# Performance work log

Hardware: AMD Instinct MI355X
Metric: run time of the kernel (lower is better)

The kernel has to match this reference:

```python
import jax, jax.numpy as jnp
import numpy as np

B, S = 2, 2048
HID, NH, NKV, HD = 4096, 32, 8, 128
THETA = 10000.0
WINDOW = 1024  # sliding window size


def setup_inputs() -> dict:
    key = jax.random.key(0)
    k1, k2, k3 = jax.random.split(key, 3)
    hidden_states = jax.random.normal(k1, (B, S, HID), jnp.float32)
    wqkv = jax.random.normal(k2, (HID, (NH + 2 * NKV) * HD), jnp.float32) * 0.02
    wo = jax.random.normal(k3, (NH * HD, HID), jnp.float32) * 0.02
    positions = jnp.arange(S, dtype=jnp.int32)
    return {"hidden_states": hidden_states, "wqkv": wqkv, "wo": wo, "positions": positions}


def _rope_neox(x, positions):
    # x: [B, S, h, HD]; GPT-NeoX style: rotate concatenated halves.
    half = HD // 2
    inv_freq = 1.0 / (THETA ** (jnp.arange(half, dtype=jnp.float32) / half))
    ang = positions.astype(jnp.float32)[:, None] * inv_freq  # [S, half]
    cos = jnp.cos(ang)[None, :, None, :]
    sin = jnp.sin(ang)[None, :, None, :]
    x1, x2 = jnp.split(x, 2, axis=-1)
    return jnp.concatenate([x1 * cos - x2 * sin, x2 * cos + x1 * sin], axis=-1)


def reference(hidden_states, wqkv, wo, positions):
    qkv = hidden_states @ wqkv  # [B, S, (NH+2*NKV)*HD]
    q, k, v = jnp.split(qkv, [NH * HD, NH * HD + NKV * HD], axis=-1)
    q = q.reshape(B, S, NH, HD)
    k = k.reshape(B, S, NKV, HD)
    v = v.reshape(B, S, NKV, HD)
    q = _rope_neox(q, positions)
    k = _rope_neox(k, positions)
    # GQA: each KV head serves NH // NKV query heads
    rep = NH // NKV
    k = jnp.repeat(k, rep, axis=2)  # [B, S, NH, HD]
    v = jnp.repeat(v, rep, axis=2)
    scale = HD ** -0.5
    scores = jnp.einsum('bqhd,bkhd->bhqk', q, k) * scale  # [B, NH, S, S]
    i = jnp.arange(S)[:, None]
    j = jnp.arange(S)[None, :]
    mask = (j <= i) & (i - j < WINDOW)  # causal + sliding window
    scores = jnp.where(mask[None, None], scores, jnp.float32(-1e30))
    probs = jax.nn.softmax(scores, axis=-1)
    attn = jnp.einsum('bhqk,bkhd->bqhd', probs, v).reshape(B, S, NH * HD)
    return attn @ wo  # [B, S, HID]
```

## Files before the change

kernel.cpp:

```cpp
#include <hip/hip_runtime.h>


typedef __attribute__((ext_vector_type(8))) short short8;
typedef __attribute__((ext_vector_type(4))) float f32x4;
typedef __attribute__((ext_vector_type(16))) float f32x16;
typedef __attribute__((ext_vector_type(4))) unsigned int u32x4;
typedef __attribute__((ext_vector_type(4))) unsigned short u16x4;

__device__ __forceinline__ unsigned short f2bf(float f) {
  unsigned int u = __builtin_bit_cast(unsigned int, f);
  u = u + 0x7fffu + ((u >> 16) & 1u);
  return (unsigned short)(u >> 16);
}
__device__ __forceinline__ float bf2f(unsigned short h) {
  unsigned int u = ((unsigned int)h) << 16;
  return __builtin_bit_cast(float, u);
}
__device__ __forceinline__ unsigned int cvtpk_bf16(float lo, float hi) {
  unsigned int r;
  asm("v_cvt_pk_bf16_f32 %0, %1, %2" : "=v"(r) : "v"(lo), "v"(hi));
  return r;
}

__device__ __forceinline__ void gload_lds16(const unsigned short* g, unsigned short* l) {
  __builtin_amdgcn_global_load_lds(
      (const __attribute__((address_space(1))) unsigned int*)g,
      (__attribute__((address_space(3))) unsigned int*)l, 16, 0, 0);
}

#define MFMA16(A, B, C) __builtin_amdgcn_mfma_f32_16x16x32_bf16((A), (B), (C), 0, 0, 0)
#define MFMA32(A, B, C) __builtin_amdgcn_mfma_f32_32x32x16_bf16((A), (B), (C), 0, 0, 0)
#define BC8(x) __builtin_bit_cast(short8, (x))

__global__ __launch_bounds__(256) void cvt1(const float* __restrict__ hs,
                                            const float* __restrict__ wqkv,
                                            unsigned short* __restrict__ hsb,
                                            unsigned short* __restrict__ wT) {
  const int bid = blockIdx.x;
  if (bid < 24576) {
    __shared__ float t[32][33];
    const int c0 = (bid % 192) * 32, r0 = (bid / 192) * 32;
    const int tx = threadIdx.x & 31, ty = threadIdx.x >> 5;
#pragma unroll
    for (int i = 0; i < 4; ++i)
      t[ty + i * 8][tx] = wqkv[(size_t)(r0 + ty + i * 8) * 6144 + c0 + tx];
    __syncthreads();
#pragma unroll
    for (int i = 0; i < 4; ++i)
      wT[(size_t)(c0 + ty + i * 8) * 4096 + r0 + tx] = f2bf(t[tx][ty + i * 8]);
  } else {
    const int i = ((bid - 24576) * 256 + threadIdx.x) * 4;
    f32x4 v = *(const f32x4*)(hs + i);
    u16x4 o;
#pragma unroll
    for (int j = 0; j < 4; ++j) o[j] = f2bf(v[j]);
    *(u16x4*)(hsb + i) = o;
  }
}

__global__ __launch_bounds__(256) void rope_cvtwo(unsigned short* __restrict__ qkv,
                                                  const int* __restrict__ pos,
                                                  const float* __restrict__ wo,
                                                  unsigned short* __restrict__ wT) {
  const int bid = blockIdx.x;
  if (bid < 8192) {
    const int idx = bid * 256 + threadIdx.x;
    const int d = idx & 63;
    const int hh = (idx >> 6) & 7;
    const int tok = idx >> 9;
    const int s = tok & 2047;
    unsigned short* p = qkv + (size_t)tok * 6144 + 4096 + hh * 128 + d;
    const float x1 = bf2f(p[0]);
    const float x2 = bf2f(p[64]);
    const float inv = exp2f(-(float)d * 0.2076205059304601f);
    const float ang = (float)pos[s] * inv;
    const float c = cosf(ang), sn = sinf(ang);
    p[0]  = f2bf(x1 * c - x2 * sn);
    p[64] = f2bf(x2 * c + x1 * sn);
  } else {
    __shared__ float t[32][33];
    const int b2 = bid - 8192;
    const int c0 = (b2 % 128) * 32, r0 = (b2 / 128) * 32;
    const int tx = threadIdx.x & 31, ty = threadIdx.x >> 5;
#pragma unroll
    for (int i = 0; i < 4; ++i)
      t[ty + i * 8][tx] = wo[(size_t)(r0 + ty + i * 8) * 4096 + c0 + tx];
    __syncthreads();
#pragma unroll
    for (int i = 0; i < 4; ++i)
      wT[(size_t)(c0 + ty + i * 8) * 4096 + r0 + tx] = f2bf(t[tx][ty + i * 8]);
  }
}

template <int NIF, int OUTF32>
__global__ __launch_bounds__(512, 2) void gemm256(const unsigned short* __restrict__ A,
                                                  const unsigned short* __restrict__ BT,
                                                  void* __restrict__ Cout,
                                                  int M, int N, int K) {
  constexpr int BUFE = 16384 + NIF * 4096;
  constexpr int NR = NIF + 4;
  __shared__ __align__(16) unsigned short lds[2][BUFE];
  const int tid = threadIdx.x;
  const int lane = tid & 63;
  const int w = tid >> 6;
  const int wr = w >> 2;
  const int wc = w & 3;
  const int g = lane >> 4;
  const int l15 = lane & 15;

  const int nwg = gridDim.x;
  const int cpx = nwg >> 3;
  const int bid = blockIdx.x;
  const int swz = (bid & 7) * cpx + (bid >> 3);
  const int MT = M >> 8;
  const int m0 = (swz % MT) * 256;
  const int n0 = (swz / MT) * (NIF * 64);

  const int lrow = lane >> 3;
  const int lcol = ((lane & 7) ^ lrow) * 8;
  const unsigned short* Asrc = A + (size_t)(m0 + w * 8 + lrow) * K + lcol;
  const unsigned short* Bsrc = BT + (size_t)(n0 + w * 8 + lrow) * K + lcol;

  f32x4 acc[8][NIF] = {};

  auto stage = [&](int buf, int t, int r) {
    if (r < NIF) {
      const int rb = r * 64;
      gload_lds16(Bsrc + (size_t)rb * K + t * 64,
                  &lds[buf][16384 + (rb + w * 8) * 64]);
    } else {
      const int j = r - NIF;
      const int rb = (j & 1) * 128 + ((j >> 1) & 1) * 64;
      gload_lds16(Asrc + (size_t)rb * K + t * 64,
                  &lds[buf][(rb + w * 8) * 64]);
    }
  };
  auto rdA = [&](int buf, int mi, int ks) {
    const int row = wr * 128 + mi * 16 + l15;
    const int cb = (ks * 64 + g * 16) ^ ((l15 & 7) << 4);
    return *(const u32x4*)((const char*)&lds[buf][0] + row * 128 + cb);
  };
  auto rdB = [&](int buf, int ni, int ks) {
    const int row = wc * (NIF * 16) + ni * 16 + l15;
    const int cb = (ks * 64 + g * 16) ^ ((l15 & 7) << 4);
    return *(const u32x4*)((const char*)&lds[buf][0] + 32768 + row * 128 + cb);
  };

#pragma unroll
  for (int r = 0; r < NR; ++r) stage(0, 0, r);
  asm volatile("s_waitcnt vmcnt(2)" ::: "memory");
  __builtin_amdgcn_s_barrier();

  const int NT = K >> 6;
  for (int t = 0; t < NT; ++t) {
    const int cb_ = t & 1, nb_ = cb_ ^ 1;
    const bool pre = (t + 1 < NT);
    u32x4 bfr[NIF][2];

    {
#pragma unroll
      for (int ni = 0; ni < NIF; ++ni) {
        bfr[ni][0] = rdB(cb_, ni, 0);
        bfr[ni][1] = rdB(cb_, ni, 1);
      }
      u32x4 af[3][2];
#pragma unroll
      for (int mi = 0; mi < 3; ++mi) {
        af[mi][0] = rdA(cb_, mi, 0);
        af[mi][1] = rdA(cb_, mi, 1);
      }
      if (pre) {
        stage(nb_, t + 1, 0); stage(nb_, t + 1, 1);
        if (NIF == 4) stage(nb_, t + 1, 2);
        asm volatile("s_waitcnt vmcnt(%0)" :: "i"(NIF == 4 ? 3 : 2) : "memory");
      } else {
        asm volatile("s_waitcnt vmcnt(0)" ::: "memory");
      }
      __builtin_amdgcn_s_barrier();
      __builtin_amdgcn_s_setprio(1);
#pragma unroll
      for (int mi = 0; mi < 3; ++mi)
#pragma unroll
        for (int ni = 0; ni < NIF; ++ni) {
          acc[mi][ni] = MFMA16(BC8(af[mi][0]), BC8(bfr[ni][0]), acc[mi][ni]);
          acc[mi][ni] = MFMA16(BC8(af[mi][1]), BC8(bfr[ni][1]), acc[mi][ni]);
        }
      __builtin_amdgcn_s_setprio(0);
      __builtin_amdgcn_s_barrier();
    }
    {
      u32x4 af[3][2];
#pragma unroll
      for (int mi = 0; mi < 3; ++mi) {
        af[mi][0] = rdA(cb_, 3 + mi, 0);
        af[mi][1] = rdA(cb_, 3 + mi, 1);
      }
      if (pre) {
        stage(nb_, t + 1, NR - 5); stage(nb_, t + 1, NR - 4); stage(nb_, t + 1, NR - 3);
      }
      __builtin_amdgcn_s_barrier();
      __builtin_amdgcn_s_setprio(1);
#pragma unroll
      for (int mi = 0; mi < 3; ++mi)
#pragma unroll
        for (int ni = 0; ni < NIF; ++ni) {
          acc[3 + mi][ni] = MFMA16(BC8(af[mi][0]), BC8(bfr[ni][0]), acc[3 + mi][ni]);
          acc[3 + mi][ni] = MFMA16(BC8(af[mi][1]), BC8(bfr[ni][1]), acc[3 + mi][ni]);
        }
      __builtin_amdgcn_s_setprio(0);
      __builtin_amdgcn_s_barrier();
    }
    {
      u32x4 af[2][2];
#pragma unroll
      for (int mi = 0; mi < 2; ++mi) {
        af[mi][0] = rdA(cb_, 6 + mi, 0);
        af[mi][1] = rdA(cb_, 6 + mi, 1);
      }
      if (pre) {
        stage(nb_, t + 1, NR - 2); stage(nb_, t + 1, NR - 1);
        asm volatile("s_waitcnt vmcnt(2)" ::: "memory");
      }
      __builtin_amdgcn_s_barrier();
      __builtin_amdgcn_s_setprio(1);
#pragma unroll
      for (int mi = 0; mi < 2; ++mi)
#pragma unroll
        for (int ni = 0; ni < NIF; ++ni) {
          acc[6 + mi][ni] = MFMA16(BC8(af[mi][0]), BC8(bfr[ni][0]), acc[6 + mi][ni]);
          acc[6 + mi][ni] = MFMA16(BC8(af[mi][1]), BC8(bfr[ni][1]), acc[6 + mi][ni]);
        }
      __builtin_amdgcn_s_setprio(0);
      __builtin_amdgcn_s_barrier();
    }
  }

  const int crow0 = m0 + wr * 128;
  const int ccol0 = n0 + wc * (NIF * 16);
#pragma unroll
  for (int mi = 0; mi < 8; ++mi)
#pragma unroll
    for (int ni = 0; ni < NIF; ++ni)
#pragma unroll
      for (int r = 0; r < 4; ++r) {
        const size_t idx =
            (size_t)(crow0 + mi * 16 + g * 4 + r) * N + (ccol0 + ni * 16 + l15);
        if constexpr (OUTF32) ((float*)Cout)[idx] = acc[mi][ni][r];
        else ((unsigned short*)Cout)[idx] = f2bf(acc[mi][ni][r]);
      }
}

__global__ __launch_bounds__(512, 2) void attn_kernel(const unsigned short* __restrict__ qkv,
                                                      unsigned short* __restrict__ aout,
                                                      const int* __restrict__ pos) {
  __shared__ __align__(16) unsigned short smem[35840];

  const int tid = threadIdx.x;
  const int lane = tid & 63;
  const int w = tid >> 6;
  const int hi = lane >> 5;
  const int l31 = lane & 31;
  const int q0 = blockIdx.x * 256;
  const int h = blockIdx.y;
  const int b = blockIdx.z;
  const int kh = h >> 2;
  const size_t tokbase = (size_t)b * 2048;
  const int qw0 = q0 + w * 32;
  const int qg = qw0 + l31;

  short8 qf[8];
  {
    const unsigned short* qp = qkv + (tokbase + qg) * 6144 + h * 128;
#pragma unroll
    for (int ks8 = 0; ks8 < 8; ++ks8)
      qf[ks8] = BC8(*(const u32x4*)(qp + ks8 * 16 + hi * 8));
    const float fp = (float)pos[qg];
#pragma unroll
    for (int ks8 = 0; ks8 < 4; ++ks8)
#pragma unroll
      for (int j = 0; j < 8; ++j) {
        const int d = ks8 * 16 + hi * 8 + j;
        const float x1 = bf2f((unsigned short)qf[ks8][j]);
        const float x2 = bf2f((unsigned short)qf[ks8 + 4][j]);
        const float ang = fp * exp2f(-(float)d * 0.2076205059304601f);
        float c, sn;
        __sincosf(ang, &sn, &c);
        c *= 0.12751743f; sn *= 0.12751743f;
        qf[ks8][j]     = (short)f2bf(x1 * c - x2 * sn);
        qf[ks8 + 4][j] = (short)f2bf(x2 * c + x1 * sn);
      }
  }

  const int c0key = tid >> 4, c0col = tid & 15;
  const int c1key = (tid + 512) >> 4, c1col = tid & 15;

  u32x4 kreg[2], vreg[2];
  const unsigned short* kvK = qkv + tokbase * 6144 + 4096 + kh * 128;

  const int t0 = (q0 >= 1024 ? (q0 - 1023) >> 6 : 0);
  const int t1 = (q0 + 255) >> 6;

  {
    const unsigned short* kb = kvK + (size_t)(t0 * 64) * 6144;
    kreg[0] = *(const u32x4*)(kb + (size_t)c0key * 6144 + c0col * 8);
    kreg[1] = *(const u32x4*)(kb + (size_t)c1key * 6144 + c1col * 8);
    vreg[0] = *(const u32x4*)(kb + (size_t)c0key * 6144 + 1024 + c0col * 8);
    vreg[1] = *(const u32x4*)(kb + (size_t)c1key * 6144 + 1024 + c1col * 8);
  }

  float m_run = -1e30f, l_run = 0.0f;
  f32x16 o_acc[4] = {};

  for (int kt = t0; kt <= t1; ++kt) {
    const int cur = (kt - t0) & 1;
    unsigned short* kdst = &smem[(cur)*17920];
    unsigned short* vdst = kdst + 8704;

    if (kt == t0) {
      *(u32x4*)&kdst[c0key * 136 + c0col * 8] = kreg[0];
      *(u32x4*)&kdst[c1key * 136 + c1col * 8] = kreg[1];
#pragma unroll
      for (int e = 0; e < 8; ++e) {
        const int e0 = (e + c0col) & 7;
        const int e1 = (e + c1col) & 7;
        vdst[(c0col * 8 + e0) * 72 + c0key] =
            (unsigned short)(vreg[0][e0 >> 1] >> ((e0 & 1) * 16));
        vdst[(c1col * 8 + e1) * 72 + c1key] =
            (unsigned short)(vreg[1][e1 >> 1] >> ((e1 & 1) * 16));
      }
      if (kt < t1) {
        const unsigned short* kb = kvK + (size_t)((kt + 1) * 64) * 6144;
        kreg[0] = *(const u32x4*)(kb + (size_t)c0key * 6144 + c0col * 8);
        kreg[1] = *(const u32x4*)(kb + (size_t)c1key * 6144 + c1col * 8);
        vreg[0] = *(const u32x4*)(kb + (size_t)c0key * 6144 + 1024 + c0col * 8);
        vreg[1] = *(const u32x4*)(kb + (size_t)c1key * 6144 + 1024 + c1col * 8);
      }
      __syncthreads();
    }

    if (kt < t1) {
      unsigned short* kdn = &smem[(cur ^ 1) * 17920];
      unsigned short* vdn = kdn + 8704;
      *(u32x4*)&kdn[c0key * 136 + c0col * 8] = kreg[0];
      *(u32x4*)&kdn[c1key * 136 + c1col * 8] = kreg[1];
#pragma unroll
      for (int e = 0; e < 8; ++e) {
        const int e0 = (e + c0col) & 7;
        const int e1 = (e + c1col) & 7;
        vdn[(c0col * 8 + e0) * 72 + c0key] =
            (unsigned short)(vreg[0][e0 >> 1] >> ((e0 & 1) * 16));
        vdn[(c1col * 8 + e1) * 72 + c1key] =
            (unsigned short)(vreg[1][e1 >> 1] >> ((e1 & 1) * 16));
      }
      if (kt + 2 <= t1) {
        const unsigned short* kb = kvK + (size_t)((kt + 2) * 64) * 6144;
        kreg[0] = *(const u32x4*)(kb + (size_t)c0key * 6144 + c0col * 8);
        kreg[1] = *(const u32x4*)(kb + (size_t)c1key * 6144 + c1col * 8);
        vreg[0] = *(const u32x4*)(kb + (size_t)c0key * 6144 + 1024 + c0col * 8);
        vreg[1] = *(const u32x4*)(kb + (size_t)c1key * 6144 + 1024 + c1col * 8);
      }
    }

    const int ktb = kt * 64;
    if (ktb <= qw0 + 31 && ktb + 63 >= qw0 - 1023) {
      const unsigned short* kb = &smem[cur * 17920];
      const unsigned short* vb = kb + 8704;

      f32x16 s0 = {}, s1 = {};
      const int arow = l31 * 136 + hi * 8;
#pragma unroll
      for (int ks8 = 0; ks8 < 8; ++ks8) {
        u32x4 a0 = *(const u32x4*)&kb[arow + ks8 * 16];
        u32x4 a1 = *(const u32x4*)&kb[arow + 32 * 136 + ks8 * 16];
        s0 = MFMA32(BC8(a0), qf[ks8], s0);
        s1 = MFMA32(BC8(a1), qf[ks8], s1);
      }

      float pv[32];
      const bool need_mask = !(ktb + 63 <= qw0 && ktb >= qw0 - 992);
      if (need_mask) {
#pragma unroll
        for (int r = 0; r < 16; ++r) {
          const int key0 = ktb + ((r & 3) + 8 * (r >> 2) + 4 * hi);
          const int key1 = key0 + 32;
          pv[r]      = (key0 <= qg && qg - key0 < 1024) ? s0[r] : -1e30f;
          pv[16 + r] = (key1 <= qg && qg - key1 < 1024) ? s1[r] : -1e30f;
        }
      } else {
#pragma unroll
        for (int r = 0; r < 16; ++r) {
          pv[r] = s0[r];
          pv[16 + r] = s1[r];
        }
      }

      float tm = -1e30f;
#pragma unroll
      for (int i = 0; i < 32; ++i) tm = fmaxf(tm, pv[i]);
      tm = fmaxf(tm, __shfl_xor(tm, 32, 64));
      if (__any(tm > m_run + 11.5415603f)) {
        const float mn = fmaxf(fmaxf(m_run, tm), -1e20f);
        const float scl = exp2f(m_run - mn);
#pragma unroll
        for (int d = 0; d < 4; ++d) o_acc[d] *= scl;
        l_run *= scl;
        m_run = mn;
      }
      float lsum = 0.0f;
#pragma unroll
      for (int i = 0; i < 32; ++i) {
        pv[i] = exp2f(pv[i] - m_run);
        lsum += pv[i];
      }
      l_run += lsum + __shfl_xor(lsum, 32, 64);

      u32x4 paf[4];
#pragma unroll
      for (int ks = 0; ks < 4; ++ks) {
        const int base = (ks >> 1) * 16 + (ks & 1) * 8;
        auto rA = __builtin_amdgcn_permlane32_swap(
            (int)cvtpk_bf16(pv[base + 0], pv[base + 1]),
            (int)cvtpk_bf16(pv[base + 4], pv[base + 5]), false, false);
        auto rB = __builtin_amdgcn_permlane32_swap(
            (int)cvtpk_bf16(pv[base + 2], pv[base + 3]),
            (int)cvtpk_bf16(pv[base + 6], pv[base + 7]), false, false);
        paf[ks][0] = (unsigned int)rA[0];
        paf[ks][1] = (unsigned int)rB[0];
        paf[ks][2] = (unsigned int)rA[1];
        paf[ks][3] = (unsigned int)rB[1];
      }

#pragma unroll
      for (int dblk = 0; dblk < 4; ++dblk) {
        const int vrow = (dblk * 32 + l31) * 72 + hi * 8;
#pragma unroll
        for (int ks = 0; ks < 4; ++ks) {
          u32x4 vf = *(const u32x4*)&vb[vrow + ks * 16];
          o_acc[dblk] = MFMA32(BC8(vf), BC8(paf[ks]), o_acc[dblk]);
        }
      }
    }

    __syncthreads();
  }

  const float rl = 1.0f / l_run;
  unsigned short* ob = &smem[w * 4352];
#pragma unroll
  for (int dblk = 0; dblk < 4; ++dblk)
#pragma unroll
    for (int rq = 0; rq < 4; ++rq) {
      u16x4 pk;
#pragma unroll
      for (int i = 0; i < 4; ++i) pk[i] = f2bf(o_acc[dblk][rq * 4 + i] * rl);
      *(u16x4*)&ob[l31 * 136 + dblk * 32 + rq * 8 + hi * 4] = pk;
    }
  __syncthreads();

  unsigned short* gout = aout + (tokbase + q0 + w * 32) * 4096 + h * 128;
#pragma unroll
  for (int r4 = 0; r4 < 8; ++r4) {
    const int row = r4 * 4 + (lane >> 4);
    u32x4 val = *(const u32x4*)&ob[row * 136 + (lane & 15) * 8];
    *(u32x4*)(gout + (size_t)row * 4096 + (lane & 15) * 8) = val;
  }
}

extern "C" void kernel_launch(void* const* d_in, const int* in_sizes, int n_in,
                              void* d_out, int out_size, void* d_ws, size_t ws_size,
                              hipStream_t stream) {
  (void)in_sizes; (void)n_in; (void)out_size; (void)ws_size;
  const float* hs   = (const float*)d_in[0];
  const float* wqkv = (const float*)d_in[1];
  const float* wo   = (const float*)d_in[2];
  const int*   pos  = (const int*)d_in[3];
  float* out = (float*)d_out;

  char* ws = (char*)d_ws;
  unsigned short* qkvb = (unsigned short*)ws;
  unsigned short* wT   = (unsigned short*)(ws + 50331648);
  unsigned short* hsb  = (unsigned short*)(ws + 100663296);

  cvt1<<<40960, 256, 0, stream>>>(hs, wqkv, hsb, wT);
  gemm256<3, 0><<<512, 512, 0, stream>>>(hsb, wT, qkvb, 4096, 6144, 4096);
  rope_cvtwo<<<24576, 256, 0, stream>>>(qkvb, pos, wo, wT);
  attn_kernel<<<dim3(8, 32, 2), 512, 0, stream>>>(qkvb, hsb, pos);
  gemm256<4, 1><<<256, 512, 0, stream>>>(hsb, wT, out, 4096, 4096, 4096);
}
```

Baseline: 489.0 us.

## Split GEMM into simple-sync and 4-phase pipelined variants, use natural-exp softmax

The single gemm256 template becomes two kernels. gemm_ss is used for the QKV projection: it waits for all loads, stages the whole next tile up front, and uses fewer barriers. gemm_p4 is used for the output projection: it splits each K-step into four phases of two M-subtiles, interleaving staged global loads with sched_barrier fences and explicit lgkmcnt waits. The attention kernel drops the folded log2e/sqrt(d) scale from the query RoPE and instead multiplies scores by 1/sqrt(d) and uses __expf with a rescale threshold of 8. The simpler sync in gemm_ss gives up load/compute overlap, and the extra per-score multiply adds ALU work in attention.

```diff
diff --git a/kernel.cpp b/kernel.cpp
--- a/kernel.cpp
+++ b/kernel.cpp
@@ -93,7 +93,7 @@
 }
 
 template <int NIF, int OUTF32>
-__global__ __launch_bounds__(512, 2) void gemm256(const unsigned short* __restrict__ A,
+__global__ __launch_bounds__(512, 2) void gemm_ss(const unsigned short* __restrict__ A,
                                                   const unsigned short* __restrict__ BT,
                                                   void* __restrict__ Cout,
                                                   int M, int N, int K) {
@@ -148,7 +148,154 @@
 
 #pragma unroll
   for (int r = 0; r < NR; ++r) stage(0, 0, r);
+
+  const int NT = K >> 6;
+  for (int t = 0; t < NT; ++t) {
+    const int cb_ = t & 1, nb_ = cb_ ^ 1;
+
+    asm volatile("s_waitcnt vmcnt(0)" ::: "memory");
+    __builtin_amdgcn_s_barrier();
+    asm volatile("" ::: "memory");
+    if (t + 1 < NT) {
+#pragma unroll
+      for (int r = 0; r < NR; ++r) stage(nb_, t + 1, r);
+    }
+
+    u32x4 bfr[NIF][2];
+#pragma unroll
+    for (int ni = 0; ni < NIF; ++ni) {
+      bfr[ni][0] = rdB(cb_, ni, 0);
+      bfr[ni][1] = rdB(cb_, ni, 1);
+    }
+
+    {
+      u32x4 af[3][2];
+#pragma unroll
+      for (int mi = 0; mi < 3; ++mi) {
+        af[mi][0] = rdA(cb_, mi, 0);
+        af[mi][1] = rdA(cb_, mi, 1);
+      }
+      __builtin_amdgcn_s_setprio(1);
+#pragma unroll
+      for (int mi = 0; mi < 3; ++mi)
+#pragma unroll
+        for (int ni = 0; ni < NIF; ++ni) {
+          acc[mi][ni] = MFMA16(BC8(af[mi][0]), BC8(bfr[ni][0]), acc[mi][ni]);
+          acc[mi][ni] = MFMA16(BC8(af[mi][1]), BC8(bfr[ni][1]), acc[mi][ni]);
+        }
+      __builtin_amdgcn_s_setprio(0);
+    }
+    __builtin_amdgcn_s_barrier();
+    {
+      u32x4 af[3][2];
+#pragma unroll
+      for (int mi = 0; mi < 3; ++mi) {
+        af[mi][0] = rdA(cb_, 3 + mi, 0);
+        af[mi][1] = rdA(cb_, 3 + mi, 1);
+      }
+      __builtin_amdgcn_s_setprio(1);
+#pragma unroll
+      for (int mi = 0; mi < 3; ++mi)
+#pragma unroll
+        for (int ni = 0; ni < NIF; ++ni) {
+          acc[3 + mi][ni] = MFMA16(BC8(af[mi][0]), BC8(bfr[ni][0]), acc[3 + mi][ni]);
+          acc[3 + mi][ni] = MFMA16(BC8(af[mi][1]), BC8(bfr[ni][1]), acc[3 + mi][ni]);
+        }
+      __builtin_amdgcn_s_setprio(0);
+    }
+    __builtin_amdgcn_s_barrier();
+    {
+      u32x4 af[2][2];
+#pragma unroll
+      for (int mi = 0; mi < 2; ++mi) {
+        af[mi][0] = rdA(cb_, 6 + mi, 0);
+        af[mi][1] = rdA(cb_, 6 + mi, 1);
+      }
+      __builtin_amdgcn_s_setprio(1);
+#pragma unroll
+      for (int mi = 0; mi < 2; ++mi)
+#pragma unroll
+        for (int ni = 0; ni < NIF; ++ni) {
+          acc[6 + mi][ni] = MFMA16(BC8(af[mi][0]), BC8(bfr[ni][0]), acc[6 + mi][ni]);
+          acc[6 + mi][ni] = MFMA16(BC8(af[mi][1]), BC8(bfr[ni][1]), acc[6 + mi][ni]);
+        }
+      __builtin_amdgcn_s_setprio(0);
+    }
+  }
+
+  const int crow0 = m0 + wr * 128;
+  const int ccol0 = n0 + wc * (NIF * 16);
+#pragma unroll
+  for (int mi = 0; mi < 8; ++mi)
+#pragma unroll
+    for (int ni = 0; ni < NIF; ++ni)
+#pragma unroll
+      for (int r = 0; r < 4; ++r) {
+        const size_t idx =
+            (size_t)(crow0 + mi * 16 + g * 4 + r) * N + (ccol0 + ni * 16 + l15);
+        if constexpr (OUTF32) ((float*)Cout)[idx] = acc[mi][ni][r];
+        else ((unsigned short*)Cout)[idx] = f2bf(acc[mi][ni][r]);
+      }
+}
+
+template <int NIF, int OUTF32>
+__global__ __launch_bounds__(512, 2) void gemm_p4(const unsigned short* __restrict__ A,
+                                                  const unsigned short* __restrict__ BT,
+                                                  void* __restrict__ Cout,
+                                                  int M, int N, int K) {
+  constexpr int BUFE = 16384 + NIF * 4096;
+  constexpr int NR = NIF + 4;
+  __shared__ __align__(16) unsigned short lds[2][BUFE];
+  const int tid = threadIdx.x;
+  const int lane = tid & 63;
+  const int w = tid >> 6;
+  const int wr = w >> 2;
+  const int wc = w & 3;
+  const int g = lane >> 4;
+  const int l15 = lane & 15;
+
+  const int nwg = gridDim.x;
+  const int cpx = nwg >> 3;
+  const int bid = blockIdx.x;
+  const int swz = (bid & 7) * cpx + (bid >> 3);
+  const int MT = M >> 8;
+  const int m0 = (swz % MT) * 256;
+  const int n0 = (swz / MT) * (NIF * 64);
+
+  const int lrow = lane >> 3;
+  const int lcol = ((lane & 7) ^ lrow) * 8;
+  const unsigned short* Asrc = A + (size_t)(m0 + w * 8 + lrow) * K + lcol;
+  const unsigned short* Bsrc = BT + (size_t)(n0 + w * 8 + lrow) * K + lcol;
+
+  f32x4 acc[8][NIF] = {};
+
+  auto stage = [&](int buf, int t, int r) {
+    if (r < NIF) {
+      const int rb = r * 64;
+      gload_lds16(Bsrc + (size_t)rb * K + t * 64,
+                  &lds[buf][16384 + (rb + w * 8) * 64]);
+    } else {
+      const int j = r - NIF;
+      const int rb = (j & 1) * 128 + ((j >> 1) & 1) * 64;
+      gload_lds16(Asrc + (size_t)rb * K + t * 64,
+                  &lds[buf][(rb + w * 8) * 64]);
+    }
+  };
+  auto rdA = [&](int buf, int mi, int ks) {
+    const int row = wr * 128 + mi * 16 + l15;
+    const int cb = (ks * 64 + g * 16) ^ ((l15 & 7) << 4);
+    return *(const u32x4*)((const char*)&lds[buf][0] + row * 128 + cb);
+  };
+  auto rdB = [&](int buf, int ni, int ks) {
+    const int row = wc * (NIF * 16) + ni * 16 + l15;
+    const int cb = (ks * 64 + g * 16) ^ ((l15 & 7) << 4);
+    return *(const u32x4*)((const char*)&lds[buf][0] + 32768 + row * 128 + cb);
+  };
+
+#pragma unroll
+  for (int r = 0; r < NR; ++r) stage(0, 0, r);
   asm volatile("s_waitcnt vmcnt(2)" ::: "memory");
+  __builtin_amdgcn_sched_barrier(0);
   __builtin_amdgcn_s_barrier();
 
   const int NT = K >> 6;
@@ -163,74 +310,92 @@
         bfr[ni][0] = rdB(cb_, ni, 0);
         bfr[ni][1] = rdB(cb_, ni, 1);
       }
-      u32x4 af[3][2];
-#pragma unroll
-      for (int mi = 0; mi < 3; ++mi) {
-        af[mi][0] = rdA(cb_, mi, 0);
-        af[mi][1] = rdA(cb_, mi, 1);
-      }
+      u32x4 a00 = rdA(cb_, 0, 0), a01 = rdA(cb_, 0, 1);
+      u32x4 a10 = rdA(cb_, 1, 0), a11 = rdA(cb_, 1, 1);
+      if (pre) { stage(nb_, t + 1, 0); stage(nb_, t + 1, 1); }
+      __builtin_amdgcn_sched_barrier(0);
+      __builtin_amdgcn_s_barrier();
+      asm volatile("s_waitcnt lgkmcnt(0)" ::: "memory");
+      __builtin_amdgcn_sched_barrier(0);
+      __builtin_amdgcn_s_setprio(1);
+#pragma unroll
+      for (int ni = 0; ni < NIF; ++ni) {
+        acc[0][ni] = MFMA16(BC8(a00), BC8(bfr[ni][0]), acc[0][ni]);
+        acc[0][ni] = MFMA16(BC8(a01), BC8(bfr[ni][1]), acc[0][ni]);
+        acc[1][ni] = MFMA16(BC8(a10), BC8(bfr[ni][0]), acc[1][ni]);
+        acc[1][ni] = MFMA16(BC8(a11), BC8(bfr[ni][1]), acc[1][ni]);
+      }
+      __builtin_amdgcn_s_setprio(0);
+      __builtin_amdgcn_sched_barrier(0);
+      __builtin_amdgcn_s_barrier();
+    }
+    {
+      u32x4 a00 = rdA(cb_, 2, 0), a01 = rdA(cb_, 2, 1);
+      u32x4 a10 = rdA(cb_, 3, 0), a11 = rdA(cb_, 3, 1);
       if (pre) {
-        stage(nb_, t + 1, 0); stage(nb_, t + 1, 1);
-        if (NIF == 4) stage(nb_, t + 1, 2);
-        asm volatile("s_waitcnt vmcnt(%0)" :: "i"(NIF == 4 ? 3 : 2) : "memory");
+        stage(nb_, t + 1, 2); stage(nb_, t + 1, 3);
+        asm volatile("s_waitcnt vmcnt(4)" ::: "memory");
       } else {
         asm volatile("s_waitcnt vmcnt(0)" ::: "memory");
       }
-      __builtin_amdgcn_s_barrier();
+      __builtin_amdgcn_sched_barrier(0);
+      __builtin_amdgcn_s_barrier();
+      asm volatile("s_waitcnt lgkmcnt(0)" ::: "memory");
+      __builtin_amdgcn_sched_barrier(0);
       __builtin_amdgcn_s_setprio(1);
 #pragma unroll
-      for (int mi = 0; mi < 3; ++mi)
-#pragma unroll
-        for (int ni = 0; ni < NIF; ++ni) {
-          acc[mi][ni] = MFMA16(BC8(af[mi][0]), BC8(bfr[ni][0]), acc[mi][ni]);
-          acc[mi][ni] = MFMA16(BC8(af[mi][1]), BC8(bfr[ni][1]), acc[mi][ni]);
-        }
+      for (int ni = 0; ni < NIF; ++ni) {
+        acc[2][ni] = MFMA16(BC8(a00), BC8(bfr[ni][0]), acc[2][ni]);
+        acc[2][ni] = MFMA16(BC8(a01), BC8(bfr[ni][1]), acc[2][ni]);
+        acc[3][ni] = MFMA16(BC8(a10), BC8(bfr[ni][0]), acc[3][ni]);
+        acc[3][ni] = MFMA16(BC8(a11), BC8(bfr[ni][1]), acc[3][ni]);
+      }
       __builtin_amdgcn_s_setprio(0);
+      __builtin_amdgcn_sched_barrier(0);
       __builtin_amdgcn_s_barrier();
     }
     {
-      u32x4 af[3][2];
-#pragma unroll
-      for (int mi = 0; mi < 3; ++mi) {
-        af[mi][0] = rdA(cb_, 3 + mi, 0);
-        af[mi][1] = rdA(cb_, 3 + mi, 1);
-      }
+      u32x4 a00 = rdA(cb_, 4, 0), a01 = rdA(cb_, 4, 1);
+      u32x4 a10 = rdA(cb_, 5, 0), a11 = rdA(cb_, 5, 1);
+      if (pre) { stage(nb_, t + 1, 4); stage(nb_, t + 1, 5); }
+      __builtin_amdgcn_sched_barrier(0);
+      __builtin_amdgcn_s_barrier();
+      asm volatile("s_waitcnt lgkmcnt(0)" ::: "memory");
+      __builtin_amdgcn_sched_barrier(0);
+      __builtin_amdgcn_s_setprio(1);
+#pragma unroll
+      for (int ni = 0; ni < NIF; ++ni) {
+        acc[4][ni] = MFMA16(BC8(a00), BC8(bfr[ni][0]), acc[4][ni]);
+        acc[4][ni] = MFMA16(BC8(a01), BC8(bfr[ni][1]), acc[4][ni]);
+        acc[5][ni] = MFMA16(BC8(a10), BC8(bfr[ni][0]), acc[5][ni]);
+        acc[5][ni] = MFMA16(BC8(a11), BC8(bfr[ni][1]), acc[5][ni]);
+      }
+      __builtin_amdgcn_s_setprio(0);
+      __builtin_amdgcn_sched_barrier(0);
+      __builtin_amdgcn_s_barrier();
+    }
+    {
+      u32x4 a00 = rdA(cb_, 6, 0), a01 = rdA(cb_, 6, 1);
+      u32x4 a10 = rdA(cb_, 7, 0), a11 = rdA(cb_, 7, 1);
       if (pre) {
-        stage(nb_, t + 1, NR - 5); stage(nb_, t + 1, NR - 4); stage(nb_, t + 1, NR - 3);
-      }
-      __builtin_amdgcn_s_barrier();
+        stage(nb_, t + 1, 6);
+        if (NR == 8) stage(nb_, t + 1, 7);
+        asm volatile("s_waitcnt vmcnt(2)" ::: "memory");
+      }
+      __builtin_amdgcn_sched_barrier(0);
+      __builtin_amdgcn_s_barrier();
+      asm volatile("s_waitcnt lgkmcnt(0)" ::: "memory");
+      __builtin_amdgcn_sched_barrier(0);
       __builtin_amdgcn_s_setprio(1);
 #pragma unroll
-      for (int mi = 0; mi < 3; ++mi)
-#pragma unroll
-        for (int ni = 0; ni < NIF; ++ni) {
-          acc[3 + mi][ni] = MFMA16(BC8(af[mi][0]), BC8(bfr[ni][0]), acc[3 + mi][ni]);
-          acc[3 + mi][ni] = MFMA16(BC8(af[mi][1]), BC8(bfr[ni][1]), acc[3 + mi][ni]);
-        }
+      for (int ni = 0; ni < NIF; ++ni) {
+        acc[6][ni] = MFMA16(BC8(a00), BC8(bfr[ni][0]), acc[6][ni]);
+        acc[6][ni] = MFMA16(BC8(a01), BC8(bfr[ni][1]), acc[6][ni]);
+        acc[7][ni] = MFMA16(BC8(a10), BC8(bfr[ni][0]), acc[7][ni]);
+        acc[7][ni] = MFMA16(BC8(a11), BC8(bfr[ni][1]), acc[7][ni]);
+      }
       __builtin_amdgcn_s_setprio(0);
-      __builtin_amdgcn_s_barrier();
-    }
-    {
-      u32x4 af[2][2];
-#pragma unroll
-      for (int mi = 0; mi < 2; ++mi) {
-        af[mi][0] = rdA(cb_, 6 + mi, 0);
-        af[mi][1] = rdA(cb_, 6 + mi, 1);
-      }
-      if (pre) {
-        stage(nb_, t + 1, NR - 2); stage(nb_, t + 1, NR - 1);
-        asm volatile("s_waitcnt vmcnt(2)" ::: "memory");
-      }
-      __builtin_amdgcn_s_barrier();
-      __builtin_amdgcn_s_setprio(1);
-#pragma unroll
-      for (int mi = 0; mi < 2; ++mi)
-#pragma unroll
-        for (int ni = 0; ni < NIF; ++ni) {
-          acc[6 + mi][ni] = MFMA16(BC8(af[mi][0]), BC8(bfr[ni][0]), acc[6 + mi][ni]);
-          acc[6 + mi][ni] = MFMA16(BC8(af[mi][1]), BC8(bfr[ni][1]), acc[6 + mi][ni]);
-        }
-      __builtin_amdgcn_s_setprio(0);
+      __builtin_amdgcn_sched_barrier(0);
       __builtin_amdgcn_s_barrier();
     }
   }
@@ -285,7 +450,6 @@
         const float ang = fp * exp2f(-(float)d * 0.2076205059304601f);
         float c, sn;
         __sincosf(ang, &sn, &c);
-        c *= 0.12751743f; sn *= 0.12751743f;
         qf[ks8][j]     = (short)f2bf(x1 * c - x2 * sn);
         qf[ks8 + 4][j] = (short)f2bf(x2 * c + x1 * sn);
       }
@@ -376,6 +540,7 @@
         s1 = MFMA32(BC8(a1), qf[ks8], s1);
       }
 
+      const float scale = 0.08838834764831845f;
       float pv[32];
       const bool need_mask = !(ktb + 63 <= qw0 && ktb >= qw0 - 992);
       if (need_mask) {
@@ -383,14 +548,14 @@
         for (int r = 0; r < 16; ++r) {
           const int key0 = ktb + ((r & 3) + 8 * (r >> 2) + 4 * hi);
           const int key1 = key0 + 32;
-          pv[r]      = (key0 <= qg && qg - key0 < 1024) ? s0[r] : -1e30f;
-          pv[16 + r] = (key1 <= qg && qg - key1 < 1024) ? s1[r] : -1e30f;
+          pv[r]      = (key0 <= qg && qg - key0 < 1024) ? s0[r] * scale : -1e30f;
+          pv[16 + r] = (key1 <= qg && qg - key1 < 1024) ? s1[r] * scale : -1e30f;
         }
       } else {
 #pragma unroll
         for (int r = 0; r < 16; ++r) {
-          pv[r] = s0[r];
-          pv[16 + r] = s1[r];
+          pv[r] = s0[r] * scale;
+          pv[16 + r] = s1[r] * scale;
         }
       }
 
@@ -398,9 +563,9 @@
 #pragma unroll
       for (int i = 0; i < 32; ++i) tm = fmaxf(tm, pv[i]);
       tm = fmaxf(tm, __shfl_xor(tm, 32, 64));
-      if (__any(tm > m_run + 11.5415603f)) {
+      if (__any(tm > m_run + 8.0f)) {
         const float mn = fmaxf(fmaxf(m_run, tm), -1e20f);
-        const float scl = exp2f(m_run - mn);
+        const float scl = __expf(m_run - mn);
 #pragma unroll
         for (int d = 0; d < 4; ++d) o_acc[d] *= scl;
         l_run *= scl;
@@ -409,7 +574,7 @@
       float lsum = 0.0f;
 #pragma unroll
       for (int i = 0; i < 32; ++i) {
-        pv[i] = exp2f(pv[i] - m_run);
+        pv[i] = __expf(pv[i] - m_run);
         lsum += pv[i];
       }
       l_run += lsum + __shfl_xor(lsum, 32, 64);
@@ -482,8 +647,8 @@
   unsigned short* hsb  = (unsigned short*)(ws + 100663296);
 
   cvt1<<<40960, 256, 0, stream>>>(hs, wqkv, hsb, wT);
-  gemm256<3, 0><<<512, 512, 0, stream>>>(hsb, wT, qkvb, 4096, 6144, 4096);
+  gemm_ss<3, 0><<<512, 512, 0, stream>>>(hsb, wT, qkvb, 4096, 6144, 4096);
   rope_cvtwo<<<24576, 256, 0, stream>>>(qkvb, pos, wo, wT);
   attn_kernel<<<dim3(8, 32, 2), 512, 0, stream>>>(qkvb, hsb, pos);
-  gemm256<4, 1><<<256, 512, 0, stream>>>(hsb, wT, out, 4096, 4096, 4096);
-}
+  gemm_p4<4, 1><<<256, 512, 0, stream>>>(hsb, wT, out, 4096, 4096, 4096);
+}
```

Measured after the change: 475.4 us. 1.03x faster.

## Replace pipelined GEMM with simpler K32 tile kernel and change softmax exp path

Applied to the files above, without the earlier changes.

Replaces the 64-wide-K software-pipelined GEMM with a simpler double-buffered kernel stepping K by 32, allowing 4 blocks per CU and a smaller N tile for the output projection. In attention, it removes the scale folded into the rope'd Q and applies the softmax scale per score, using natural exp instead of exp2 and a lower rescale threshold. This gains occupancy and simplicity, but loses the swizzled LDS layout and the finer-grained load/compute overlap, and adds per-score multiplies.

```diff
diff --git a/kernel.cpp b/kernel.cpp
--- a/kernel.cpp
+++ b/kernel.cpp
@@ -93,12 +93,11 @@
 }
 
 template <int NIF, int OUTF32>
-__global__ __launch_bounds__(512, 2) void gemm256(const unsigned short* __restrict__ A,
-                                                  const unsigned short* __restrict__ BT,
-                                                  void* __restrict__ Cout,
-                                                  int M, int N, int K) {
-  constexpr int BUFE = 16384 + NIF * 4096;
-  constexpr int NR = NIF + 4;
+__global__ __launch_bounds__(512, 4) void gemm_k32(const unsigned short* __restrict__ A,
+                                                   const unsigned short* __restrict__ BT,
+                                                   void* __restrict__ Cout,
+                                                   int M, int N, int K) {
+  constexpr int BUFE = 8192 + NIF * 2048;
   __shared__ __align__(16) unsigned short lds[2][BUFE];
   const int tid = threadIdx.x;
   const int lane = tid & 63;
@@ -116,123 +115,56 @@
   const int m0 = (swz % MT) * 256;
   const int n0 = (swz / MT) * (NIF * 64);
 
-  const int lrow = lane >> 3;
-  const int lcol = ((lane & 7) ^ lrow) * 8;
-  const unsigned short* Asrc = A + (size_t)(m0 + w * 8 + lrow) * K + lcol;
-  const unsigned short* Bsrc = BT + (size_t)(n0 + w * 8 + lrow) * K + lcol;
+  const int lr = lane >> 2;
+  const int lq = (lane & 3) * 8;
+  const unsigned short* Asrc = A + (size_t)(m0 + lr) * K + lq;
+  const unsigned short* Bsrc = BT + (size_t)(n0 + lr) * K + lq;
 
   f32x4 acc[8][NIF] = {};
 
-  auto stage = [&](int buf, int t, int r) {
-    if (r < NIF) {
-      const int rb = r * 64;
-      gload_lds16(Bsrc + (size_t)rb * K + t * 64,
-                  &lds[buf][16384 + (rb + w * 8) * 64]);
-    } else {
-      const int j = r - NIF;
-      const int rb = (j & 1) * 128 + ((j >> 1) & 1) * 64;
-      gload_lds16(Asrc + (size_t)rb * K + t * 64,
-                  &lds[buf][(rb + w * 8) * 64]);
+  auto stage = [&](int buf, int t) {
+    const int tc = t * 32;
+    gload_lds16(Asrc + (size_t)(w * 16) * K + tc, &lds[buf][w * 512]);
+    gload_lds16(Asrc + (size_t)(128 + w * 16) * K + tc, &lds[buf][4096 + w * 512]);
+    gload_lds16(Bsrc + (size_t)(w * 16) * K + tc, &lds[buf][8192 + w * 512]);
+    if constexpr (NIF == 3) {
+      if (w < 4)
+        gload_lds16(Bsrc + (size_t)(128 + w * 16) * K + tc,
+                    &lds[buf][12288 + w * 512]);
     }
   };
-  auto rdA = [&](int buf, int mi, int ks) {
+  auto rdA = [&](int buf, int mi) {
     const int row = wr * 128 + mi * 16 + l15;
-    const int cb = (ks * 64 + g * 16) ^ ((l15 & 7) << 4);
-    return *(const u32x4*)((const char*)&lds[buf][0] + row * 128 + cb);
+    return *(const u32x4*)&lds[buf][row * 32 + g * 8];
   };
-  auto rdB = [&](int buf, int ni, int ks) {
+  auto rdB = [&](int buf, int ni) {
     const int row = wc * (NIF * 16) + ni * 16 + l15;
-    const int cb = (ks * 64 + g * 16) ^ ((l15 & 7) << 4);
-    return *(const u32x4*)((const char*)&lds[buf][0] + 32768 + row * 128 + cb);
+    return *(const u32x4*)&lds[buf][8192 + row * 32 + g * 8];
   };
 
-#pragma unroll
-  for (int r = 0; r < NR; ++r) stage(0, 0, r);
-  asm volatile("s_waitcnt vmcnt(2)" ::: "memory");
-  __builtin_amdgcn_s_barrier();
-
-  const int NT = K >> 6;
+  stage(0, 0);
+
+  const int NT = K >> 5;
   for (int t = 0; t < NT; ++t) {
     const int cb_ = t & 1, nb_ = cb_ ^ 1;
-    const bool pre = (t + 1 < NT);
-    u32x4 bfr[NIF][2];
-
-    {
-#pragma unroll
-      for (int ni = 0; ni < NIF; ++ni) {
-        bfr[ni][0] = rdB(cb_, ni, 0);
-        bfr[ni][1] = rdB(cb_, ni, 1);
-      }
-      u32x4 af[3][2];
-#pragma unroll
-      for (int mi = 0; mi < 3; ++mi) {
-        af[mi][0] = rdA(cb_, mi, 0);
-        af[mi][1] = rdA(cb_, mi, 1);
-      }
-      if (pre) {
-        stage(nb_, t + 1, 0); stage(nb_, t + 1, 1);
-        if (NIF == 4) stage(nb_, t + 1, 2);
-        asm volatile("s_waitcnt vmcnt(%0)" :: "i"(NIF == 4 ? 3 : 2) : "memory");
-      } else {
-        asm volatile("s_waitcnt vmcnt(0)" ::: "memory");
-      }
-      __builtin_amdgcn_s_barrier();
-      __builtin_amdgcn_s_setprio(1);
-#pragma unroll
-      for (int mi = 0; mi < 3; ++mi)
-#pragma unroll
-        for (int ni = 0; ni < NIF; ++ni) {
-          acc[mi][ni] = MFMA16(BC8(af[mi][0]), BC8(bfr[ni][0]), acc[mi][ni]);
-          acc[mi][ni] = MFMA16(BC8(af[mi][1]), BC8(bfr[ni][1]), acc[mi][ni]);
-        }
-      __builtin_amdgcn_s_setprio(0);
-      __builtin_amdgcn_s_barrier();
-    }
-    {
-      u32x4 af[3][2];
-#pragma unroll
-      for (int mi = 0; mi < 3; ++mi) {
-        af[mi][0] = rdA(cb_, 3 + mi, 0);
-        af[mi][1] = rdA(cb_, 3 + mi, 1);
-      }
-      if (pre) {
-        stage(nb_, t + 1, NR - 5); stage(nb_, t + 1, NR - 4); stage(nb_, t + 1, NR - 3);
-      }
-      __builtin_amdgcn_s_barrier();
-      __builtin_amdgcn_s_setprio(1);
-#pragma unroll
-      for (int mi = 0; mi < 3; ++mi)
-#pragma unroll
-        for (int ni = 0; ni < NIF; ++ni) {
-          acc[3 + mi][ni] = MFMA16(BC8(af[mi][0]), BC8(bfr[ni][0]), acc[3 + mi][ni]);
-          acc[3 + mi][ni] = MFMA16(BC8(af[mi][1]), BC8(bfr[ni][1]), acc[3 + mi][ni]);
-        }
-      __builtin_amdgcn_s_setprio(0);
-      __builtin_amdgcn_s_barrier();
-    }
-    {
-      u32x4 af[2][2];
-#pragma unroll
-      for (int mi = 0; mi < 2; ++mi) {
-        af[mi][0] = rdA(cb_, 6 + mi, 0);
-        af[mi][1] = rdA(cb_, 6 + mi, 1);
-      }
-      if (pre) {
-        stage(nb_, t + 1, NR - 2); stage(nb_, t + 1, NR - 1);
-        asm volatile("s_waitcnt vmcnt(2)" ::: "memory");
-      }
-      __builtin_amdgcn_s_barrier();
-      __builtin_amdgcn_s_setprio(1);
-#pragma unroll
-      for (int mi = 0; mi < 2; ++mi)
-#pragma unroll
-        for (int ni = 0; ni < NIF; ++ni) {
-          acc[6 + mi][ni] = MFMA16(BC8(af[mi][0]), BC8(bfr[ni][0]), acc[6 + mi][ni]);
-          acc[6 + mi][ni] = MFMA16(BC8(af[mi][1]), BC8(bfr[ni][1]), acc[6 + mi][ni]);
-        }
-      __builtin_amdgcn_s_setprio(0);
-      __builtin_amdgcn_s_barrier();
-    }
+
+    asm volatile("s_waitcnt vmcnt(0)" ::: "memory");
+    __builtin_amdgcn_s_barrier();
+    asm volatile("" ::: "memory");
+    if (t + 1 < NT) stage(nb_, t + 1);
+
+    u32x4 bf[NIF];
+#pragma unroll
+    for (int ni = 0; ni < NIF; ++ni) bf[ni] = rdB(cb_, ni);
+    __builtin_amdgcn_s_setprio(1);
+#pragma unroll
+    for (int mi = 0; mi < 8; ++mi) {
+      u32x4 a = rdA(cb_, mi);
+#pragma unroll
+      for (int ni = 0; ni < NIF; ++ni)
+        acc[mi][ni] = MFMA16(BC8(a), BC8(bf[ni]), acc[mi][ni]);
+    }
+    __builtin_amdgcn_s_setprio(0);
   }
 
   const int crow0 = m0 + wr * 128;
@@ -285,7 +217,6 @@
         const float ang = fp * exp2f(-(float)d * 0.2076205059304601f);
         float c, sn;
         __sincosf(ang, &sn, &c);
-        c *= 0.12751743f; sn *= 0.12751743f;
         qf[ks8][j]     = (short)f2bf(x1 * c - x2 * sn);
         qf[ks8 + 4][j] = (short)f2bf(x2 * c + x1 * sn);
       }
@@ -376,6 +307,7 @@
         s1 = MFMA32(BC8(a1), qf[ks8], s1);
       }
 
+      const float scale = 0.08838834764831845f;
       float pv[32];
       const bool need_mask = !(ktb + 63 <= qw0 && ktb >= qw0 - 992);
       if (need_mask) {
@@ -383,14 +315,14 @@
         for (int r = 0; r < 16; ++r) {
           const int key0 = ktb + ((r & 3) + 8 * (r >> 2) + 4 * hi);
           const int key1 = key0 + 32;
-          pv[r]      = (key0 <= qg && qg - key0 < 1024) ? s0[r] : -1e30f;
-          pv[16 + r] = (key1 <= qg && qg - key1 < 1024) ? s1[r] : -1e30f;
+          pv[r]      = (key0 <= qg && qg - key0 < 1024) ? s0[r] * scale : -1e30f;
+          pv[16 + r] = (key1 <= qg && qg - key1 < 1024) ? s1[r] * scale : -1e30f;
         }
       } else {
 #pragma unroll
         for (int r = 0; r < 16; ++r) {
-          pv[r] = s0[r];
-          pv[16 + r] = s1[r];
+          pv[r] = s0[r] * scale;
+          pv[16 + r] = s1[r] * scale;
         }
       }
 
@@ -398,9 +330,9 @@
 #pragma unroll
       for (int i = 0; i < 32; ++i) tm = fmaxf(tm, pv[i]);
       tm = fmaxf(tm, __shfl_xor(tm, 32, 64));
-      if (__any(tm > m_run + 11.5415603f)) {
+      if (__any(tm > m_run + 8.0f)) {
         const float mn = fmaxf(fmaxf(m_run, tm), -1e20f);
-        const float scl = exp2f(m_run - mn);
+        const float scl = __expf(m_run - mn);
 #pragma unroll
         for (int d = 0; d < 4; ++d) o_acc[d] *= scl;
         l_run *= scl;
@@ -409,7 +341,7 @@
       float lsum = 0.0f;
 #pragma unroll
       for (int i = 0; i < 32; ++i) {
-        pv[i] = exp2f(pv[i] - m_run);
+        pv[i] = __expf(pv[i] - m_run);
         lsum += pv[i];
       }
       l_run += lsum + __shfl_xor(lsum, 32, 64);
@@ -482,8 +414,8 @@
   unsigned short* hsb  = (unsigned short*)(ws + 100663296);
 
   cvt1<<<40960, 256, 0, stream>>>(hs, wqkv, hsb, wT);
-  gemm256<3, 0><<<512, 512, 0, stream>>>(hsb, wT, qkvb, 4096, 6144, 4096);
+  gemm_k32<3, 0><<<512, 512, 0, stream>>>(hsb, wT, qkvb, 4096, 6144, 4096);
   rope_cvtwo<<<24576, 256, 0, stream>>>(qkvb, pos, wo, wT);
   attn_kernel<<<dim3(8, 32, 2), 512, 0, stream>>>(qkvb, hsb, pos);
-  gemm256<4, 1><<<256, 512, 0, stream>>>(hsb, wT, out, 4096, 4096, 4096);
-}
+  gemm_k32<2, 1><<<512, 512, 0, stream>>>(hsb, wT, out, 4096, 4096, 4096);
+}
```

New measurement: 492.2 us. No clear change (+0.6%).
